# Kernel optimization log

Measured on AMD Instinct MI355X. Metric: run time of the kernel, lower is better.

The kernel has to match this reference:

```python
import jax, jax.numpy as jnp
from jax import lax
import numpy as np

OUT_CH = 16      # texture_features
INTER = 32       # texture_features_intermediate
TEXDIM = 1024    # texture_dimensions
IN_SIZE = 76


def _leaky(x):
    return jnp.where(x >= 0, x, 0.02 * x)


def grid_sample_bilinear_border(tex, grid):
    """torch.nn.functional.grid_sample, mode='bilinear', padding_mode='border',
    align_corners=False.  tex: (N,C,H,W); grid: (N,Ho,Wo,2) with (x,y) in [-1,1].
    N == 1 here; vectorized over H,W via fancy indexing."""
    N, C, H, W = tex.shape
    x, y = grid[..., 0], grid[..., 1]
    # unnormalize (align_corners=False)
    ix = ((x + 1.0) * W - 1.0) * 0.5
    iy = ((y + 1.0) * H - 1.0) * 0.5
    # border padding: clamp continuous coords
    ix = jnp.clip(ix, 0.0, W - 1.0)
    iy = jnp.clip(iy, 0.0, H - 1.0)
    x0 = jnp.floor(ix); y0 = jnp.floor(iy)
    wx = ix - x0; wy = iy - y0
    x0i = jnp.clip(x0, 0, W - 1).astype(jnp.int32)
    x1i = jnp.clip(x0 + 1, 0, W - 1).astype(jnp.int32)
    y0i = jnp.clip(y0, 0, H - 1).astype(jnp.int32)
    y1i = jnp.clip(y0 + 1, 0, H - 1).astype(jnp.int32)
    t = tex[0]  # (C,H,W)
    v00 = t[:, y0i[0], x0i[0]]  # (C,Ho,Wo)
    v01 = t[:, y0i[0], x1i[0]]
    v10 = t[:, y1i[0], x0i[0]]
    v11 = t[:, y1i[0], x1i[0]]
    wx = wx[0][None]; wy = wy[0][None]  # (1,Ho,Wo) broadcast over C
    out = (v00 * (1 - wx) * (1 - wy) + v01 * wx * (1 - wy)
           + v10 * (1 - wx) * wy + v11 * wx * wy)
    return out[None]  # (1,C,Ho,Wo)


def setup_inputs() -> dict:
    key = jax.random.key(0)
    ks = jax.random.split(key, 11)
    expressions = jax.random.normal(ks[0], (1, IN_SIZE), jnp.float32)
    audio_features = jax.random.normal(ks[1], (1, 16), jnp.float32)
    uv_inputs = jax.random.uniform(ks[2], (1, 2, 1024, 1024), jnp.float32, -1.0, 1.0)
    data = jax.random.normal(ks[3], (1, INTER, TEXDIM, TEXDIM), jnp.float32)
    def lin(kw, kb, fo, fi):
        s = 1.0 / np.sqrt(fi).astype(np.float32)
        return (jax.random.uniform(kw, (fo, fi), jnp.float32, -s, s),
                jax.random.uniform(kb, (fo,), jnp.float32, -s, s))
    W1, b1 = lin(ks[4], ks[5], 128, IN_SIZE)
    W2, b2 = lin(ks[6], ks[7], 64, 128)
    W3, b3 = lin(ks[8], ks[9], OUT_CH * 4 * 4 * INTER, 64)
    return {"expressions": expressions, "audio_features": audio_features,
            "uv_inputs": uv_inputs, "data": data,
            "W1": W1, "b1": b1, "W2": W2, "b2": b2, "W3": W3, "b3": b3}


def reference(expressions, audio_features, uv_inputs, data, W1, b1, W2, b2, W3, b3):
    # tiny MLP -> dynamic 4x4 conv filter
    h = expressions.reshape(1, 1, -1)
    h = _leaky(h @ W1.T + b1)
    h = _leaky(h @ W2.T + b2)
    f = jnp.tanh(h @ W3.T + b3)
    conv_filter = f.reshape(OUT_CH, INTER, 4, 4)
    # conv2d(data, filter, stride=1, padding=2) -> (1, OUT_CH, D+1, D+1)
    tex_eval = lax.conv_general_dilated(
        data, conv_filter, window_strides=(1, 1), padding=((2, 2), (2, 2)),
        dimension_numbers=("NCHW", "OIHW", "NCHW"))
    # grid: stack x (chan 0) and y (chan 1) along last dim
    grid = jnp.stack([uv_inputs[:, 0], uv_inputs[:, 1]], axis=3)  # (1,Ho,Wo,2)
    return grid_sample_bilinear_border(tex_eval, grid)
```

## Files before the change

### kernel.cpp

```cpp
#include <hip/hip_runtime.h>
#include <math.h>

#define NPX   1048576
#define TD    1025
#define PW    35
#define PH    19
#define DPAD  1028
#define ROWB  65792
#define DP_OFF 33673216

typedef _Float16 half8 __attribute__((ext_vector_type(8)));
typedef _Float16 half4 __attribute__((ext_vector_type(4)));
typedef float    f32x4 __attribute__((ext_vector_type(4)));

__device__ __forceinline__ void load_lds16(const void* g, void* lds) {
    __builtin_amdgcn_global_load_lds(
        (const __attribute__((address_space(1))) void*)g,
        (__attribute__((address_space(3))) void*)lds, 16, 0, 0);
}

__global__ __launch_bounds__(256) void mlp_kernel(
    const float* __restrict__ expr,
    const float* __restrict__ W1, const float* __restrict__ b1,
    const float* __restrict__ W2, const float* __restrict__ b2,
    const float* __restrict__ W3, const float* __restrict__ b3,
    _Float16* __restrict__ ffrag_g)
{
    __shared__ float sx[76];
    __shared__ float sh1[128];
    __shared__ float sh2[64];
    int t = threadIdx.x;
    if (t < 76) sx[t] = expr[t];
    __syncthreads();
    if (t < 128) {
        float a = b1[t];
        const float* w = W1 + t * 76;
        #pragma unroll 4
        for (int i = 0; i < 76; ++i) a += sx[i] * w[i];
        sh1[t] = a >= 0.f ? a : 0.02f * a;
    }
    __syncthreads();
    if (t < 64) {
        float a = b2[t];
        const float* w = W2 + t * 128;
        #pragma unroll 4
        for (int i = 0; i < 128; ++i) a += sh1[i] * w[i];
        sh2[t] = a >= 0.f ? a : 0.02f * a;
    }
    __syncthreads();
    int o = blockIdx.x * 256 + t;
    float a = b3[o];
    const float* w = W3 + o * 64;
    #pragma unroll 4
    for (int i = 0; i < 64; ++i) a += sh2[i] * w[i];
    a = tanhf(a);
    int oc = o >> 9;
    int ic = (o >> 4) & 31;
    int kk = o & 15;
    ffrag_g[(size_t)(kk * 64 + (ic >> 3) * 16 + oc) * 8 + (ic & 7)] = (_Float16)a;
}

__global__ __launch_bounds__(256) void repack_kernel(
    const float* __restrict__ data, _Float16* __restrict__ Dp)
{
    __shared__ _Float16 s[256 * 32];
    int tid = threadIdx.x;
    int Y = blockIdx.y;
    int X = blockIdx.x * 256 + tid;
    int y = Y - 2, x = X - 2;
    bool ok = ((unsigned)y < 1024u) && ((unsigned)x < 1024u);
    const float* dp = data + ((size_t)y << 10) + x;

    float v[32];
    #pragma unroll
    for (int j = 0; j < 32; ++j) v[j] = 0.f;
    if (ok) {
        #pragma unroll
        for (int j = 0; j < 32; ++j) v[j] = __builtin_nontemporal_load(&dp[(size_t)j * NPX]);
    }
    #pragma unroll
    for (int g = 0; g < 4; ++g) {
        half8 h;
        #pragma unroll
        for (int j = 0; j < 8; ++j) h[j] = (_Float16)v[g * 8 + j];
        int chunk = tid * 4 + g;
        int sw = chunk ^ ((chunk >> 3) & 7);
        *(half8*)((char*)s + sw * 16) = h;
    }
    __syncthreads();
    char* rowbase = (char*)Dp + (size_t)Y * ROWB + blockIdx.x * 16384;
    int lim = ROWB - blockIdx.x * 16384;
    #pragma unroll
    for (int i = 0; i < 4; ++i) {
        int off = tid * 16 + i * 4096;
        if (off < lim) {
            int chunk = tid + i * 256;
            int sw = chunk ^ ((chunk >> 3) & 7);
            *(uint4*)(rowbase + off) = *(uint4*)((char*)s + sw * 16);
        }
    }
}

__global__ __launch_bounds__(256, 3) void conv_mfma_kernel(
    const _Float16* __restrict__ Dp,
    const _Float16* __restrict__ ffrag_g,
    _Float16* __restrict__ tex)
{
    __shared__ __attribute__((aligned(128))) _Float16 sp[PH * PW * 32];

    int tid = threadIdx.x;
    int l = tid & 63, w = tid >> 6;
    int ox0 = blockIdx.x * 32;
    int oy0 = blockIdx.y * 16;

    half8 bfrag[16];
    #pragma unroll
    for (int kk = 0; kk < 16; ++kk)
        bfrag[kk] = *(const half8*)&ffrag_g[kk * 512 + l * 8];

    int lsw = l ^ ((l >> 3) & 7);
    for (int r = w; r < PH; r += 4) {
        int gy = min(oy0 + r, DPAD - 1);
        const char* grow = (const char*)Dp + (size_t)gy * ROWB;
        _Float16* lrow = sp + r * (PW * 32);
        #pragma unroll
        for (int c = 0; c < 3; ++c) {
            int off = ox0 * 64 + c * 1024 + lsw * 16;
            off = min(off, ROWB - 16);
            if (c < 2 || l < 12)
                load_lds16(grow + off, (char*)lrow + c * 1024);
        }
    }
    __syncthreads();

    int lane15 = l & 15;
    int q = l >> 4;

    int u = lane15 * 4 + q;
    int sv[4];
    #pragma unroll
    for (int kx = 0; kx < 4; ++kx) {
        int vch = kx * 4 + u;
        sv[kx] = (vch ^ ((vch >> 3) & 7)) * 16;
    }

    f32x4 acc[8];
    #pragma unroll
    for (int t = 0; t < 8; ++t) acc[t] = (f32x4){0.f, 0.f, 0.f, 0.f};

    #pragma unroll 4
    for (int kk = 0; kk < 16; ++kk) {
        int ky = kk >> 2, kx = kk & 3;
        #pragma unroll
        for (int t = 0; t < 8; ++t) {
            const char* ap = (const char*)sp
                + (w * 4 + (t >> 1) + ky) * (PW * 64)
                + (t & 1) * 1024 + sv[kx];
            half8 af = *(const half8*)ap;
            acc[t] = __builtin_amdgcn_mfma_f32_16x16x32_f16(bfrag[kk], af, acc[t], 0, 0, 0);
        }
    }

    #pragma unroll
    for (int t = 0; t < 8; ++t) {
        int oy = oy0 + w * 4 + (t >> 1);
        int px = ox0 + (t & 1) * 16 + lane15;
        if (oy > 1024 || px > 1024) continue;
        half4 hv;
        #pragma unroll
        for (int r = 0; r < 4; ++r) hv[r] = (_Float16)acc[t][r];
        *(half4*)&tex[((size_t)oy * TD + px) * 16 + q * 4] = hv;
    }
}

__global__ __launch_bounds__(256, 6) void sample_kernel(
    const float* __restrict__ uv,
    const _Float16* __restrict__ tex,
    float* __restrict__ out)
{
    int p = blockIdx.x * 256 + threadIdx.x;
    float x = __builtin_nontemporal_load(&uv[p]);
    float y = __builtin_nontemporal_load(&uv[NPX + p]);
    float ix = fminf(fmaxf(((x + 1.f) * 1025.f - 1.f) * 0.5f, 0.f), 1024.f);
    float iy = fminf(fmaxf(((y + 1.f) * 1025.f - 1.f) * 0.5f, 0.f), 1024.f);
    float fx0 = floorf(ix), fy0 = floorf(iy);
    float wx = ix - fx0, wy = iy - fy0;
    int x0 = (int)fx0, y0 = (int)fy0;
    int x1 = min(x0 + 1, 1024), y1 = min(y0 + 1, 1024);

    const half8* t00 = (const half8*)(tex + ((size_t)y0 * TD + x0) * 16);
    const half8* t01 = (const half8*)(tex + ((size_t)y0 * TD + x1) * 16);
    const half8* t10 = (const half8*)(tex + ((size_t)y1 * TD + x0) * 16);
    const half8* t11 = (const half8*)(tex + ((size_t)y1 * TD + x1) * 16);

    half8 v0 = t00[0], v1 = t00[1];
    half8 v2 = t01[0], v3 = t01[1];
    half8 v4 = t10[0], v5 = t10[1];
    half8 v6 = t11[0], v7 = t11[1];

    float w00 = (1.f - wx) * (1.f - wy);
    float w01 = wx * (1.f - wy);
    float w10 = (1.f - wx) * wy;
    float w11 = wx * wy;

    #pragma unroll
    for (int c = 0; c < 8; ++c) {
        float r0 = (float)v0[c] * w00 + (float)v2[c] * w01
                 + (float)v4[c] * w10 + (float)v6[c] * w11;
        float r1 = (float)v1[c] * w00 + (float)v3[c] * w01
                 + (float)v5[c] * w10 + (float)v7[c] * w11;
        __builtin_nontemporal_store(r0, &out[(size_t)c * NPX + p]);
        __builtin_nontemporal_store(r1, &out[(size_t)(c + 8) * NPX + p]);
    }
}

extern "C" void kernel_launch(void* const* d_in, const int* in_sizes, int n_in,
                              void* d_out, int out_size, void* d_ws, size_t ws_size,
                              hipStream_t stream) {
    const float* expr = (const float*)d_in[0];
    const float* uv   = (const float*)d_in[2];
    const float* data = (const float*)d_in[3];
    const float* W1   = (const float*)d_in[4];
    const float* b1   = (const float*)d_in[5];
    const float* W2   = (const float*)d_in[6];
    const float* b2   = (const float*)d_in[7];
    const float* W3   = (const float*)d_in[8];
    const float* b3   = (const float*)d_in[9];
    float* out = (float*)d_out;

    _Float16* ffrag_g  = (_Float16*)d_ws;
    _Float16* tex      = (_Float16*)((char*)d_ws + 49152);
    _Float16* Dp       = (_Float16*)((char*)d_ws + DP_OFF);

    mlp_kernel<<<32, 256, 0, stream>>>(expr, W1, b1, W2, b2, W3, b3, ffrag_g);
    repack_kernel<<<dim3(5, DPAD), 256, 0, stream>>>(data, Dp);
    conv_mfma_kernel<<<dim3(33, 65), 256, 0, stream>>>(Dp, ffrag_g, tex);
    sample_kernel<<<NPX / 256, 256, 0, stream>>>(uv, tex, out);
}
```

Measured before the change: 365.0 us.

## Store texel pairs contiguously and halve conv tile height for occupancy

The conv kernel now writes each texel into a doubled-width texture layout that holds pixel x and x+1 side by side (32 halves per entry). The sampler can then fetch each bilinear row pair with one contiguous 64-byte read instead of two separate 32-byte reads. The conv tile also shrinks to 8 output rows per block, with a smaller LDS patch and 6 blocks per CU, to raise occupancy. The cost is twice the texture footprint and redundant writes from the conv kernel, plus more halo reloading per block.

```diff
diff --git a/kernel.cpp b/kernel.cpp
--- a/kernel.cpp
+++ b/kernel.cpp
@@ -4,10 +4,10 @@
 #define NPX   1048576
 #define TD    1025
 #define PW    35
-#define PH    19
+#define PH    11
 #define DPAD  1028
 #define ROWB  65792
-#define DP_OFF 33673216
+#define DP_OFF 67289152
 
 typedef _Float16 half8 __attribute__((ext_vector_type(8)));
 typedef _Float16 half4 __attribute__((ext_vector_type(4)));
@@ -101,7 +101,7 @@
     }
 }
 
-__global__ __launch_bounds__(256, 3) void conv_mfma_kernel(
+__global__ __launch_bounds__(256, 6) void conv_mfma_kernel(
     const _Float16* __restrict__ Dp,
     const _Float16* __restrict__ ffrag_g,
     _Float16* __restrict__ tex)
@@ -111,7 +111,7 @@
     int tid = threadIdx.x;
     int l = tid & 63, w = tid >> 6;
     int ox0 = blockIdx.x * 32;
-    int oy0 = blockIdx.y * 16;
+    int oy0 = blockIdx.y * 8;
 
     half8 bfrag[16];
     #pragma unroll
@@ -144,17 +144,17 @@
         sv[kx] = (vch ^ ((vch >> 3) & 7)) * 16;
     }
 
-    f32x4 acc[8];
-    #pragma unroll
-    for (int t = 0; t < 8; ++t) acc[t] = (f32x4){0.f, 0.f, 0.f, 0.f};
+    f32x4 acc[4];
+    #pragma unroll
+    for (int t = 0; t < 4; ++t) acc[t] = (f32x4){0.f, 0.f, 0.f, 0.f};
 
     #pragma unroll 4
     for (int kk = 0; kk < 16; ++kk) {
         int ky = kk >> 2, kx = kk & 3;
         #pragma unroll
-        for (int t = 0; t < 8; ++t) {
+        for (int t = 0; t < 4; ++t) {
             const char* ap = (const char*)sp
-                + (w * 4 + (t >> 1) + ky) * (PW * 64)
+                + (w * 2 + (t >> 1) + ky) * (PW * 64)
                 + (t & 1) * 1024 + sv[kx];
             half8 af = *(const half8*)ap;
             acc[t] = __builtin_amdgcn_mfma_f32_16x16x32_f16(bfrag[kk], af, acc[t], 0, 0, 0);
@@ -162,14 +162,19 @@
     }
 
     #pragma unroll
-    for (int t = 0; t < 8; ++t) {
-        int oy = oy0 + w * 4 + (t >> 1);
+    for (int t = 0; t < 4; ++t) {
+        int oy = oy0 + w * 2 + (t >> 1);
         int px = ox0 + (t & 1) * 16 + lane15;
         if (oy > 1024 || px > 1024) continue;
         half4 hv;
         #pragma unroll
         for (int r = 0; r < 4; ++r) hv[r] = (_Float16)acc[t][r];
-        *(half4*)&tex[((size_t)oy * TD + px) * 16 + q * 4] = hv;
+        size_t base = ((size_t)oy * TD + px) * 32;
+        *(half4*)&tex[base + q * 4] = hv;
+        if (px > 0)
+            *(half4*)&tex[base - 16 + q * 4] = hv;
+        if (px == 1024)
+            *(half4*)&tex[base + 16 + q * 4] = hv;
     }
 }
 
@@ -186,17 +191,15 @@
     float fx0 = floorf(ix), fy0 = floorf(iy);
     float wx = ix - fx0, wy = iy - fy0;
     int x0 = (int)fx0, y0 = (int)fy0;
-    int x1 = min(x0 + 1, 1024), y1 = min(y0 + 1, 1024);
-
-    const half8* t00 = (const half8*)(tex + ((size_t)y0 * TD + x0) * 16);
-    const half8* t01 = (const half8*)(tex + ((size_t)y0 * TD + x1) * 16);
-    const half8* t10 = (const half8*)(tex + ((size_t)y1 * TD + x0) * 16);
-    const half8* t11 = (const half8*)(tex + ((size_t)y1 * TD + x1) * 16);
-
-    half8 v0 = t00[0], v1 = t00[1];
-    half8 v2 = t01[0], v3 = t01[1];
-    half8 v4 = t10[0], v5 = t10[1];
-    half8 v6 = t11[0], v7 = t11[1];
+    int y1 = min(y0 + 1, 1024);
+
+    const half8* r0 = (const half8*)(tex + ((size_t)y0 * TD + x0) * 32);
+    const half8* r1 = (const half8*)(tex + ((size_t)y1 * TD + x0) * 32);
+
+    half8 v0 = r0[0], v1 = r0[1];
+    half8 v2 = r0[2], v3 = r0[3];
+    half8 v4 = r1[0], v5 = r1[1];
+    half8 v6 = r1[2], v7 = r1[3];
 
     float w00 = (1.f - wx) * (1.f - wy);
     float w01 = wx * (1.f - wy);
@@ -205,12 +208,12 @@
 
     #pragma unroll
     for (int c = 0; c < 8; ++c) {
-        float r0 = (float)v0[c] * w00 + (float)v2[c] * w01
-                 + (float)v4[c] * w10 + (float)v6[c] * w11;
-        float r1 = (float)v1[c] * w00 + (float)v3[c] * w01
-                 + (float)v5[c] * w10 + (float)v7[c] * w11;
-        __builtin_nontemporal_store(r0, &out[(size_t)c * NPX + p]);
-        __builtin_nontemporal_store(r1, &out[(size_t)(c + 8) * NPX + p]);
+        float r0v = (float)v0[c] * w00 + (float)v2[c] * w01
+                  + (float)v4[c] * w10 + (float)v6[c] * w11;
+        float r1v = (float)v1[c] * w00 + (float)v3[c] * w01
+                  + (float)v5[c] * w10 + (float)v7[c] * w11;
+        __builtin_nontemporal_store(r0v, &out[(size_t)c * NPX + p]);
+        __builtin_nontemporal_store(r1v, &out[(size_t)(c + 8) * NPX + p]);
     }
 }
 
@@ -229,11 +232,11 @@
     float* out = (float*)d_out;
 
     _Float16* ffrag_g  = (_Float16*)d_ws;
-    _Float16* tex      = (_Float16*)((char*)d_ws + 49152);
+    _Float16* tex2     = (_Float16*)((char*)d_ws + 49152);
     _Float16* Dp       = (_Float16*)((char*)d_ws + DP_OFF);
 
     mlp_kernel<<<32, 256, 0, stream>>>(expr, W1, b1, W2, b2, W3, b3, ffrag_g);
     repack_kernel<<<dim3(5, DPAD), 256, 0, stream>>>(data, Dp);
-    conv_mfma_kernel<<<dim3(33, 65), 256, 0, stream>>>(Dp, ffrag_g, tex);
-    sample_kernel<<<NPX / 256, 256, 0, stream>>>(uv, tex, out);
-}
+    conv_mfma_kernel<<<dim3(33, 129), 256, 0, stream>>>(Dp, ffrag_g, tex2);
+    sample_kernel<<<NPX / 256, 256, 0, stream>>>(uv, tex2, out);
+}
```

Result: slower. 396.9 us (+8.7%).
